# Kernel optimization log

Hardware: AMD Instinct MI355X
Metric: run time of the kernel (lower is better)

## Reference

```python
import jax, jax.numpy as jnp
import numpy as np

B, G, C, H = 32, 512, 384, 768
TAU = 0.1
ITERS = 10


def _xavier(key, shape):
    fan_in, fan_out = shape
    lim = (6.0 / (fan_in + fan_out)) ** 0.5
    return jax.random.uniform(key, shape, minval=-lim, maxval=lim, dtype=jnp.float32)


def setup_inputs() -> dict:
    key = jax.random.key(0)
    ks = jax.random.split(key, 4)
    return {
        "center_coords": jax.random.normal(ks[0], (B, G, 3), dtype=jnp.float32),
        "group_features": jax.random.normal(ks[1], (B, G, C), dtype=jnp.float32),
        "W1": _xavier(ks[2], (C, H)),
        "b1": jnp.zeros((H,), jnp.float32),
        "W2": _xavier(ks[3], (H, G)),
        "b2": jnp.zeros((G,), jnp.float32),
    }


def _sinkhorn(scores):
    # scores: (B, G, G); log-space Sinkhorn row/col normalization
    log_alpha = scores / TAU
    for _ in range(ITERS):
        log_alpha = log_alpha - jax.nn.logsumexp(log_alpha, axis=-1, keepdims=True)
        log_alpha = log_alpha - jax.nn.logsumexp(log_alpha, axis=-2, keepdims=True)
    return jnp.exp(log_alpha)


def _greedy_assign(P):
    # Equivalent to torch loop: process entries in descending value order,
    # assign (row, col) if both free == repeatedly take global argmax over
    # entries with free row and free col. P: (G, G) -> perm: (G,) int32.
    g = P.shape[-1]
    flat = P.reshape(-1)

    def step(_, carry):
        row_free, col_free, assign = carry
        mask = (row_free[:, None] & col_free[None, :]).reshape(-1)
        idx = jnp.argmax(jnp.where(mask, flat, -jnp.inf))
        r = idx // g
        c = idx % g
        return (row_free.at[r].set(False), col_free.at[c].set(False), assign.at[r].set(c.astype(jnp.int32)))

    init = (jnp.ones((g,), bool), jnp.ones((g,), bool), jnp.full((g,), -1, jnp.int32))
    _, _, assign = jax.lax.fori_loop(0, g, step, init)
    return assign


def _apply_perm(data, perm):
    # reordered[new_pos] = data[orig_pos]; perm[orig_pos] = new_pos
    return jnp.zeros_like(data).at[perm].set(data)


def reference(center_coords, group_features, W1, b1, W2, b2):
    h = jax.nn.relu(jnp.einsum('bgc,ch->bgh', group_features, W1) + b1)
    scores = jnp.einsum('bgh,hk->bgk', h, W2) + b2  # (B, G, G)
    P = _sinkhorn(scores)
    perm_indices = jax.vmap(_greedy_assign)(P)  # (B, G)
    reordered_coords = jax.vmap(_apply_perm)(center_coords, perm_indices)
    reordered_feats = jax.vmap(_apply_perm)(group_features, perm_indices)
    return reordered_coords, reordered_feats, perm_indices
```

## Files before the change

### kernel.cpp

```cpp
#include <hip/hip_runtime.h>
#include <math.h>

#define NB 32
#define NG 512
#define NC 384
#define NH 768

typedef float f32x4v __attribute__((ext_vector_type(4)));
typedef __bf16 bf16_t;
typedef bf16_t bf16x8 __attribute__((ext_vector_type(8)));
typedef bf16_t bf16x4 __attribute__((ext_vector_type(4)));

#define LDSK 32

__device__ __forceinline__ void split3(float x, bf16_t& h, bf16_t& m, bf16_t& lo)
{
    h = (bf16_t)x;
    float r1 = x - (float)h;
    m = (bf16_t)r1;
    float r2 = r1 - (float)m;
    lo = (bf16_t)r2;
}

__global__ __launch_bounds__(256, 4) void gemm_bias_mfma(
    const float* __restrict__ A, const float* __restrict__ Bw,
    const float* __restrict__ bias, float* __restrict__ Co,
    int M, int N, int K, int mode)
{
    __shared__ __align__(16) bf16_t sA[3][128][LDSK];
    __shared__ __align__(16) bf16_t sB[3][64][LDSK];
    int ntiles = N >> 6;
    int bm = (blockIdx.x / ntiles) << 7;
    int bn = (blockIdx.x % ntiles) << 6;
    int t = threadIdx.x;
    int l = t & 63;
    int w = t >> 6;
    int wr = (w >> 1) << 6;
    int wc = (w & 1) << 5;
    int fr = l & 15;
    int fk = (l >> 4) << 3;

    int sa_row = t >> 1;
    int sa_kh = (t & 1) << 4;
    int hsel = (sa_kh >> 4) << 2;
    int sb_k = (t & 7) << 2;
    int sb_n = ((t >> 3) & 15) << 2;
    bool doB = t < 128;
    int bcol = ((sb_k >> 2) & 3) * 8 + ((sb_k >> 4) << 2);

    const float* apBase = A + (size_t)(bm + sa_row) * K + sa_kh;

    f32x4v acc[4][2];
#pragma unroll
    for (int i = 0; i < 4; i++)
#pragma unroll
        for (int j = 0; j < 2; j++) acc[i][j] = (f32x4v)(0.f);

    float4 q0 = *(const float4*)(apBase + 0);
    float4 q1 = *(const float4*)(apBase + 4);
    float4 q2 = *(const float4*)(apBase + 8);
    float4 q3 = *(const float4*)(apBase + 12);
    float4 bq0, bq1, bq2, bq3;
    if (doB) {
        bq0 = *(const float4*)(Bw + (size_t)(sb_k + 0) * N + bn + sb_n);
        bq1 = *(const float4*)(Bw + (size_t)(sb_k + 1) * N + bn + sb_n);
        bq2 = *(const float4*)(Bw + (size_t)(sb_k + 2) * N + bn + sb_n);
        bq3 = *(const float4*)(Bw + (size_t)(sb_k + 3) * N + bn + sb_n);
    }

    for (int kc = 0; kc < K; kc += 32) {
        __syncthreads();
        {
            float xs[16] = { q0.x, q0.y, q0.z, q0.w, q1.x, q1.y, q1.z, q1.w,
                             q2.x, q2.y, q2.z, q2.w, q3.x, q3.y, q3.z, q3.w };
            bf16_t hs[16], ms[16], ls[16];
#pragma unroll
            for (int e = 0; e < 16; e++) split3(xs[e], hs[e], ms[e], ls[e]);
#pragma unroll
            for (int qd = 0; qd < 4; qd++) {
                int col = qd * 8 + hsel;
                *(bf16x4*)&sA[0][sa_row][col] =
                    (bf16x4){ hs[4 * qd], hs[4 * qd + 1], hs[4 * qd + 2], hs[4 * qd + 3] };
                *(bf16x4*)&sA[1][sa_row][col] =
                    (bf16x4){ ms[4 * qd], ms[4 * qd + 1], ms[4 * qd + 2], ms[4 * qd + 3] };
                *(bf16x4*)&sA[2][sa_row][col] =
                    (bf16x4){ ls[4 * qd], ls[4 * qd + 1], ls[4 * qd + 2], ls[4 * qd + 3] };
            }
        }
        if (doB) {
            float bbv[4][4] = {
                { bq0.x, bq0.y, bq0.z, bq0.w },
                { bq1.x, bq1.y, bq1.z, bq1.w },
                { bq2.x, bq2.y, bq2.z, bq2.w },
                { bq3.x, bq3.y, bq3.z, bq3.w } };
#pragma unroll
            for (int n = 0; n < 4; n++) {
                bf16_t hb[4], mb[4], lb[4];
#pragma unroll
                for (int kk = 0; kk < 4; kk++) split3(bbv[kk][n], hb[kk], mb[kk], lb[kk]);
                *(bf16x4*)&sB[0][sb_n + n][bcol] = (bf16x4){ hb[0], hb[1], hb[2], hb[3] };
                *(bf16x4*)&sB[1][sb_n + n][bcol] = (bf16x4){ mb[0], mb[1], mb[2], mb[3] };
                *(bf16x4*)&sB[2][sb_n + n][bcol] = (bf16x4){ lb[0], lb[1], lb[2], lb[3] };
            }
        }
        __syncthreads();
        if (kc + 32 < K) {
            const float* ap = apBase + kc + 32;
            q0 = *(const float4*)(ap + 0);
            q1 = *(const float4*)(ap + 4);
            q2 = *(const float4*)(ap + 8);
            q3 = *(const float4*)(ap + 12);
            if (doB) {
                const float* bp = Bw + (size_t)(kc + 32 + sb_k) * N + bn + sb_n;
                bq0 = *(const float4*)(bp + 0 * N);
                bq1 = *(const float4*)(bp + 1 * N);
                bq2 = *(const float4*)(bp + 2 * N);
                bq3 = *(const float4*)(bp + 3 * N);
            }
        }
        bf16x8 afH[4], afM[4], afL[4], bfH[2], bfM[2], bfL[2];
#pragma unroll
        for (int i = 0; i < 4; i++) {
            afH[i] = *(const bf16x8*)&sA[0][wr + i * 16 + fr][fk];
            afM[i] = *(const bf16x8*)&sA[1][wr + i * 16 + fr][fk];
            afL[i] = *(const bf16x8*)&sA[2][wr + i * 16 + fr][fk];
        }
#pragma unroll
        for (int j = 0; j < 2; j++) {
            bfH[j] = *(const bf16x8*)&sB[0][wc + j * 16 + fr][fk];
            bfM[j] = *(const bf16x8*)&sB[1][wc + j * 16 + fr][fk];
            bfL[j] = *(const bf16x8*)&sB[2][wc + j * 16 + fr][fk];
        }
#pragma unroll
        for (int i = 0; i < 4; i++)
#pragma unroll
            for (int j = 0; j < 2; j++) {
                acc[i][j] = __builtin_amdgcn_mfma_f32_16x16x32_bf16(
                    afH[i], bfH[j], acc[i][j], 0, 0, 0);
                acc[i][j] = __builtin_amdgcn_mfma_f32_16x16x32_bf16(
                    afH[i], bfM[j], acc[i][j], 0, 0, 0);
                acc[i][j] = __builtin_amdgcn_mfma_f32_16x16x32_bf16(
                    afM[i], bfH[j], acc[i][j], 0, 0, 0);
                acc[i][j] = __builtin_amdgcn_mfma_f32_16x16x32_bf16(
                    afM[i], bfM[j], acc[i][j], 0, 0, 0);
                acc[i][j] = __builtin_amdgcn_mfma_f32_16x16x32_bf16(
                    afH[i], bfL[j], acc[i][j], 0, 0, 0);
                acc[i][j] = __builtin_amdgcn_mfma_f32_16x16x32_bf16(
                    afL[i], bfH[j], acc[i][j], 0, 0, 0);
            }
    }

    int orow = (l >> 4) << 2;
#pragma unroll
    for (int j = 0; j < 2; j++) {
        int colg = bn + wc + j * 16 + fr;
        float bj = bias[colg];
#pragma unroll
        for (int i = 0; i < 4; i++) {
            int rowg = bm + wr + i * 16 + orow;
#pragma unroll
            for (int r = 0; r < 4; r++) {
                float val = acc[i][j][r] + bj;
                val = (mode == 0) ? fmaxf(val, 0.f) : val / 0.1f;
                Co[(size_t)(rowg + r) * N + colg] = val;
            }
        }
    }
}

#define DPP6_MAXF(x)                                                              \
    { int _t;                                                                     \
      _t = __builtin_amdgcn_update_dpp(__float_as_int(x), __float_as_int(x),      \
               0x111, 0xf, 0xf, false); x = fmaxf(x, __int_as_float(_t));         \
      _t = __builtin_amdgcn_update_dpp(__float_as_int(x), __float_as_int(x),      \
               0x112, 0xf, 0xf, false); x = fmaxf(x, __int_as_float(_t));         \
      _t = __builtin_amdgcn_update_dpp(__float_as_int(x), __float_as_int(x),      \
               0x114, 0xf, 0xf, false); x = fmaxf(x, __int_as_float(_t));         \
      _t = __builtin_amdgcn_update_dpp(__float_as_int(x), __float_as_int(x),      \
               0x118, 0xf, 0xf, false); x = fmaxf(x, __int_as_float(_t));         \
      _t = __builtin_amdgcn_update_dpp(__float_as_int(x), __float_as_int(x),      \
               0x142, 0xa, 0xf, false); x = fmaxf(x, __int_as_float(_t));         \
      _t = __builtin_amdgcn_update_dpp(__float_as_int(x), __float_as_int(x),      \
               0x143, 0xc, 0xf, false); x = fmaxf(x, __int_as_float(_t)); }

#define DPP6_ADDF(x)                                                              \
    { int _t;                                                                     \
      _t = __builtin_amdgcn_update_dpp(__float_as_int(x), __float_as_int(x),      \
               0x111, 0xf, 0xf, false); x = x + __int_as_float(_t);               \
      _t = __builtin_amdgcn_update_dpp(__float_as_int(x), __float_as_int(x),      \
               0x112, 0xf, 0xf, false); x = x + __int_as_float(_t);               \
      _t = __builtin_amdgcn_update_dpp(__float_as_int(x), __float_as_int(x),      \
               0x114, 0xf, 0xf, false); x = x + __int_as_float(_t);               \
      _t = __builtin_amdgcn_update_dpp(__float_as_int(x), __float_as_int(x),      \
               0x118, 0xf, 0xf, false); x = x + __int_as_float(_t);               \
      _t = __builtin_amdgcn_update_dpp(__float_as_int(x), __float_as_int(x),      \
               0x142, 0xa, 0xf, false); x = x + __int_as_float(_t);               \
      _t = __builtin_amdgcn_update_dpp(__float_as_int(x), __float_as_int(x),      \
               0x143, 0xc, 0xf, false); x = x + __int_as_float(_t); }

__global__ __launch_bounds__(256) void sinkhorn_iter(
    const float* __restrict__ A0, float* __restrict__ uu,
    const float* __restrict__ vv, float* __restrict__ ps)
{
    int blk = blockIdx.x;
    int b = blk >> 3, rc = blk & 7;
    int t = threadIdx.x;
    int l = t & 63, w = t >> 6;
    const float* vb = vv + (b << 9);
    float4 v0 = *(const float4*)(vb + 4 * l);
    float4 v1 = *(const float4*)(vb + 256 + 4 * l);
    int row0 = (rc << 6) + (w << 4);
    const float* base = A0 + ((size_t)((b << 9) + row0) << 9);

    float cs0 = 0.f, cs1 = 0.f, cs2 = 0.f, cs3 = 0.f;
    float cs4 = 0.f, cs5 = 0.f, cs6 = 0.f, cs7 = 0.f;

    for (int rr = 0; rr < 16; ++rr) {
        const float* rowp = base + ((size_t)rr << 9);
        float4 a0 = *(const float4*)(rowp + 4 * l);
        float4 a1 = *(const float4*)(rowp + 256 + 4 * l);
        float x0 = a0.x + v0.x, x1 = a0.y + v0.y;
        float x2 = a0.z + v0.z, x3 = a0.w + v0.w;
        float x4 = a1.x + v1.x, x5 = a1.y + v1.y;
        float x6 = a1.z + v1.z, x7 = a1.w + v1.w;
        float m = fmaxf(fmaxf(fmaxf(x0, x1), fmaxf(x2, x3)),
                        fmaxf(fmaxf(x4, x5), fmaxf(x6, x7)));
        DPP6_MAXF(m)
        int mi = __builtin_amdgcn_readlane(__float_as_int(m), 63);
        m = __int_as_float(mi);
        float e0 = __expf(x0 - m), e1 = __expf(x1 - m);
        float e2 = __expf(x2 - m), e3 = __expf(x3 - m);
        float e4 = __expf(x4 - m), e5 = __expf(x5 - m);
        float e6 = __expf(x6 - m), e7 = __expf(x7 - m);
        float s = ((e0 + e1) + (e2 + e3)) + ((e4 + e5) + (e6 + e7));
        DPP6_ADDF(s)
        int si = __builtin_amdgcn_readlane(__float_as_int(s), 63);
        s = __int_as_float(si);
        float inv = 1.0f / s;
        cs0 += e0 * inv; cs1 += e1 * inv; cs2 += e2 * inv; cs3 += e3 * inv;
        cs4 += e4 * inv; cs5 += e5 * inv; cs6 += e6 * inv; cs7 += e7 * inv;
        if (l == 63) uu[(b << 9) + row0 + rr] = -(m + __logf(s));
    }

    __shared__ float sacc[4][512];
    float4 w0; w0.x = cs0; w0.y = cs1; w0.z = cs2; w0.w = cs3;
    float4 w1; w1.x = cs4; w1.y = cs5; w1.z = cs6; w1.w = cs7;
    *(float4*)&sacc[w][4 * l] = w0;
    *(float4*)&sacc[w][256 + 4 * l] = w1;
    __syncthreads();
    float pA = sacc[0][t] + sacc[1][t] + sacc[2][t] + sacc[3][t];
    float pB = sacc[0][256 + t] + sacc[1][256 + t] + sacc[2][256 + t] + sacc[3][256 + t];
    int o = ((b << 3) + rc) * NG;
    ps[o + t] = pA;
    ps[o + 256 + t] = pB;
}

__global__ __launch_bounds__(256) void col_combine_lin(
    const float* __restrict__ ps, float* __restrict__ vv)
{
    int tid = blockIdx.x * 256 + threadIdx.x;
    int b = tid >> 9, j = tid & 511;
    float S = 0.f;
#pragma unroll
    for (int rc = 0; rc < 8; rc++) S += ps[((b << 3) + rc) * NG + j];
    vv[tid] = vv[tid] - __logf(S);
}

__device__ __forceinline__ void masked_row_argmax(
    const float* __restrict__ rowp, int l, unsigned int free8, int rr,
    float& outV, int& outF)
{
    float4 x0 = *(const float4*)(rowp + 8 * l);
    float4 x1 = *(const float4*)(rowp + 8 * l + 4);
    float q0 = (free8 & 1u)   ? x0.x : -1.0f;
    float q1 = (free8 & 2u)   ? x0.y : -1.0f;
    float q2 = (free8 & 4u)   ? x0.z : -1.0f;
    float q3 = (free8 & 8u)   ? x0.w : -1.0f;
    float q4 = (free8 & 16u)  ? x1.x : -1.0f;
    float q5 = (free8 & 32u)  ? x1.y : -1.0f;
    float q6 = (free8 & 64u)  ? x1.z : -1.0f;
    float q7 = (free8 & 128u) ? x1.w : -1.0f;
    float lm = fmaxf(fmaxf(fmaxf(q0, q1), fmaxf(q2, q3)),
                     fmaxf(fmaxf(q4, q5), fmaxf(q6, q7)));
    int sb = (rr << 9) + 8 * l;
    int lf = 0x7FFFFFFF;
    lf = (q7 == lm) ? sb + 7 : lf;
    lf = (q6 == lm) ? sb + 6 : lf;
    lf = (q5 == lm) ? sb + 5 : lf;
    lf = (q4 == lm) ? sb + 4 : lf;
    lf = (q3 == lm) ? sb + 3 : lf;
    lf = (q2 == lm) ? sb + 2 : lf;
    lf = (q1 == lm) ? sb + 1 : lf;
    lf = (q0 == lm) ? sb + 0 : lf;
    float gg = lm;
    DPP6_MAXF(gg)
    int ggi = __builtin_amdgcn_readlane(__float_as_int(gg), 63);
    float g1 = __int_as_float(ggi);
    unsigned long long tb = __ballot(lm == g1);
    int tl = __ffsll(tb) - 1;
    outV = g1;
    outF = __builtin_amdgcn_readlane(lf, tl);
}

__global__ __launch_bounds__(256) void p_rowmax(
    const float* __restrict__ A0, const float* __restrict__ uu,
    const float* __restrict__ vv, float* __restrict__ P,
    int* __restrict__ rbCr, int* __restrict__ rbCc,
    unsigned long long* __restrict__ freeRow,
    unsigned long long* __restrict__ freeCol,
    int* __restrict__ remaining)
{
    if (blockIdx.x == 0) {
        int t = threadIdx.x;
        freeRow[t] = ~0ULL;
        freeCol[t] = ~0ULL;
        if (t < NB) remaining[t] = NG;
    }
    int wrow = blockIdx.x * 4 + (threadIdx.x >> 6);
    int l = threadIdx.x & 63;
    int b = wrow >> 9;
    float ur = uu[wrow];
    const float* vb = vv + (b << 9);
    size_t ro = (size_t)wrow << 9;
    float4 a0 = *(const float4*)(A0 + ro + 8 * l);
    float4 a1 = *(const float4*)(A0 + ro + 8 * l + 4);
    float4 v0 = *(const float4*)(vb + 8 * l);
    float4 v1 = *(const float4*)(vb + 8 * l + 4);
    float p0 = expf(a0.x + ur + v0.x);
    float p1 = expf(a0.y + ur + v0.y);
    float p2 = expf(a0.z + ur + v0.z);
    float p3 = expf(a0.w + ur + v0.w);
    float p4 = expf(a1.x + ur + v1.x);
    float p5 = expf(a1.y + ur + v1.y);
    float p6 = expf(a1.z + ur + v1.z);
    float p7 = expf(a1.w + ur + v1.w);
    float4 o0; o0.x = p0; o0.y = p1; o0.z = p2; o0.w = p3;
    float4 o1; o1.x = p4; o1.y = p5; o1.z = p6; o1.w = p7;
    *(float4*)(P + ro + 8 * l) = o0;
    *(float4*)(P + ro + 8 * l + 4) = o1;
    float mv = fmaxf(fmaxf(fmaxf(p0, p1), fmaxf(p2, p3)),
                     fmaxf(fmaxf(p4, p5), fmaxf(p6, p7)));
    int cb = 8 * l;
    int f = 0x7FFFFFFF;
    f = (p7 == mv) ? cb + 7 : f;
    f = (p6 == mv) ? cb + 6 : f;
    f = (p5 == mv) ? cb + 5 : f;
    f = (p4 == mv) ? cb + 4 : f;
    f = (p3 == mv) ? cb + 3 : f;
    f = (p2 == mv) ? cb + 2 : f;
    f = (p1 == mv) ? cb + 1 : f;
    f = (p0 == mv) ? cb + 0 : f;
    float g = mv;
    DPP6_MAXF(g)
    int gi = __builtin_amdgcn_readlane(__float_as_int(g), 63);
    float gm = __int_as_float(gi);
    unsigned long long tb = __ballot(mv == gm);
    int tl = __ffsll(tb) - 1;
    int bestc = __builtin_amdgcn_readlane(f, tl);
    if (l == 0) { rbCr[wrow] = bestc; rbCc[wrow] = -1; }
}

__global__ __launch_bounds__(512) void mutual_round(
    const float* __restrict__ P, int* __restrict__ rbCr, int* __restrict__ rbCc,
    unsigned long long* __restrict__ freeRow,
    unsigned long long* __restrict__ freeCol,
    int* __restrict__ remaining, int* __restrict__ permInt)
{
    int b = blockIdx.x;
    if (remaining[b] == 0) return;
    int t = threadIdx.x;
    int l = t & 63;
    int w = t >> 6;
    const float* Pb = P + (size_t)b * NG * NG;

    __shared__ unsigned int fr[16], fc[16];
    __shared__ int sRC[NG];
    __shared__ int sCC[NG];
    __shared__ int freeList[NG];
    __shared__ int dirtyRows[NG];
    __shared__ int nFree, nDirtyRow, takeCnt;
    __shared__ int wCnt[8], wOff[8];

    if (t < 8) {
        unsigned long long x = freeRow[b * 8 + t];
        fr[2 * t] = (unsigned)x; fr[2 * t + 1] = (unsigned)(x >> 32);
    } else if (t < 16) {
        int i = t - 8;
        unsigned long long x = freeCol[b * 8 + i];
        fc[2 * i] = (unsigned)x; fc[2 * i + 1] = (unsigned)(x >> 32);
    }
    sRC[t] = rbCr[(b << 9) + t];
    sCC[t] = rbCc[(b << 9) + t];
    if (t == 0) { nDirtyRow = 0; takeCnt = 0; }
    __syncthreads();

    bool isFree = (fr[t >> 5] >> (t & 31)) & 1u;
    unsigned long long bm = __ballot(isFree);
    if (l == 0) wCnt[w] = __popcll(bm);
    if (isFree) {
        int c = sRC[t];
        if (!((fc[c >> 5] >> (c & 31)) & 1u)) {
            int d = atomicAdd(&nDirtyRow, 1);
            dirtyRows[d] = t;
        }
    }
    __syncthreads();
    if (t == 0) {
        int s = 0;
#pragma unroll
        for (int i = 0; i < 8; i++) { wOff[i] = s; s += wCnt[i]; }
        nFree = s;
    }
    __syncthreads();
    if (isFree) {
        int rank = __popcll(bm & ((1ULL << l) - 1ULL));
        freeList[wOff[w] + rank] = t;
    }
    __syncthreads();

    int nd = nDirtyRow;
    for (int d = w; d < nd; d += 8) {
        int r = dirtyRows[d];
        unsigned int free8 = (fc[l >> 2] >> ((l & 3) * 8)) & 0xFFu;
        float nv; int nf;
        masked_row_argmax(Pb + ((size_t)r << 9), l, free8, r, nv, nf);
        if (l == 0) {
            int c = nf & 511;
            sRC[r] = c;
            rbCr[(b << 9) + r] = c;
        }
    }
    __syncthreads();

    bool colFree = (fc[t >> 5] >> (t & 31)) & 1u;
    int cachedR = sCC[t];
    bool colDirty = colFree &&
        (cachedR < 0 || !((fr[cachedR >> 5] >> (cachedR & 31)) & 1u));
    if (colDirty) {
        float best = -1.f; int bestr = 0x7FFFFFFF;
        int nf2 = nFree;
        int i = 0;
        for (; i + 4 <= nf2; i += 4) {
            int r0 = freeList[i], r1 = freeList[i + 1];
            int r2 = freeList[i + 2], r3 = freeList[i + 3];
            float v0 = Pb[((size_t)r0 << 9) + t];
            float v1 = Pb[((size_t)r1 << 9) + t];
            float v2 = Pb[((size_t)r2 << 9) + t];
            float v3 = Pb[((size_t)r3 << 9) + t];
            if (v0 > best) { best = v0; bestr = r0; }
            if (v1 > best) { best = v1; bestr = r1; }
            if (v2 > best) { best = v2; bestr = r2; }
            if (v3 > best) { best = v3; bestr = r3; }
        }
        for (; i < nf2; ++i) {
            int ri = freeList[i];
            float vv2 = Pb[((size_t)ri << 9) + t];
            if (vv2 > best) { best = vv2; bestr = ri; }
        }
        sCC[t] = bestr;
        rbCc[(b << 9) + t] = bestr;
    }
    __syncthreads();

    if (colFree) {
        int r = sCC[t];
        if (r >= 0 && r < NG && sRC[r] == t) {
            permInt[(b << 9) + r] = t;
            atomicAnd(&fr[r >> 5], ~(1u << (r & 31)));
            atomicAnd(&fc[t >> 5], ~(1u << (t & 31)));
            atomicAdd(&takeCnt, 1);
        }
    }
    __syncthreads();
    if (t < 8) {
        freeRow[b * 8 + t] =
            ((unsigned long long)fr[2 * t + 1] << 32) | fr[2 * t];
    } else if (t < 16) {
        int i = t - 8;
        freeCol[b * 8 + i] =
            ((unsigned long long)fc[2 * i + 1] << 32) | fc[2 * i];
    }
    if (t == 0) remaining[b] = remaining[b] - takeCnt;
}

__global__ __launch_bounds__(64) void greedy_cleanup(
    const float* __restrict__ P,
    const unsigned long long* __restrict__ freeRow,
    const unsigned long long* __restrict__ freeCol,
    const int* __restrict__ remaining, int* __restrict__ permInt)
{
    int b = blockIdx.x;
    if (remaining[b] == 0) return;
    int l = threadIdx.x;
    const float* Pb = P + (size_t)b * NG * NG;

    unsigned long long wR = freeRow[b * 8 + (l >> 3)];
    unsigned int myRows = (unsigned int)((wR >> ((l & 7) * 8)) & 0xFF);
    unsigned long long wC = freeCol[b * 8 + (l >> 3)];
    unsigned int free8 = (unsigned int)((wC >> ((l & 7) * 8)) & 0xFF);

    float rv[8]; int rf[8];
#pragma unroll
    for (int k = 0; k < 8; k++) { rv[k] = -1.f; rf[k] = 0x7FFFFFFF; }

    int dmk = (int)myRows;
    unsigned long long act = __ballot(dmk != 0);
    while (act) {
        int src = __ffsll(act) - 1;
        int kk = __ffs(__builtin_amdgcn_readlane(dmk, src)) - 1;
        if (l == src) dmk &= ~(1 << kk);
        int rr = (src << 3) + kk;
        float nv; int nf;
        masked_row_argmax(Pb + ((size_t)rr << 9), l, free8, rr, nv, nf);
        bool upd = (l == src);
        rv[0] = (upd && kk == 0) ? nv : rv[0]; rf[0] = (upd && kk == 0) ? nf : rf[0];
        rv[1] = (upd && kk == 1) ? nv : rv[1]; rf[1] = (upd && kk == 1) ? nf : rf[1];
        rv[2] = (upd && kk == 2) ? nv : rv[2]; rf[2] = (upd && kk == 2) ? nf : rf[2];
        rv[3] = (upd && kk == 3) ? nv : rv[3]; rf[3] = (upd && kk == 3) ? nf : rf[3];
        rv[4] = (upd && kk == 4) ? nv : rv[4]; rf[4] = (upd && kk == 4) ? nf : rf[4];
        rv[5] = (upd && kk == 5) ? nv : rv[5]; rf[5] = (upd && kk == 5) ? nf : rf[5];
        rv[6] = (upd && kk == 6) ? nv : rv[6]; rf[6] = (upd && kk == 6) ? nf : rf[6];
        rv[7] = (upd && kk == 7) ? nv : rv[7]; rf[7] = (upd && kk == 7) ? nf : rf[7];
        act = __ballot(dmk != 0);
    }

    for (int step = 0; step < NG; ++step) {
        float mv = fmaxf(fmaxf(fmaxf(rv[0], rv[1]), fmaxf(rv[2], rv[3])),
                         fmaxf(fmaxf(rv[4], rv[5]), fmaxf(rv[6], rv[7])));
        int f = 0x7FFFFFFF;
        f = (rv[7] == mv) ? rf[7] : f;
        f = (rv[6] == mv) ? rf[6] : f;
        f = (rv[5] == mv) ? rf[5] : f;
        f = (rv[4] == mv) ? rf[4] : f;
        f = (rv[3] == mv) ? rf[3] : f;
        f = (rv[2] == mv) ? rf[2] : f;
        f = (rv[1] == mv) ? rf[1] : f;
        f = (rv[0] == mv) ? rf[0] : f;
        float g = mv;
        DPP6_MAXF(g)
        int gi = __builtin_amdgcn_readlane(__float_as_int(g), 63);
        float gm = __int_as_float(gi);
        if (gm < 0.f) break;
        unsigned long long tb = __ballot(mv == gm);
        int tl = __ffsll(tb) - 1;
        int bestf = __builtin_amdgcn_readlane(f, tl);
        int r = bestf >> 9, c = bestf & 511;
        if (l == 0) permInt[(b << 9) + r] = c;
        if (l == (c >> 3)) free8 &= ~(1u << (c & 7));
        int rl = r - (l << 3);
        int dm2 = 0;
#pragma unroll
        for (int k = 0; k < 8; k++) {
            bool alive = rv[k] >= 0.f;
            bool cm = ((rf[k] ^ c) & 511) == 0;
            bool taken = (rl == k);
            if (taken) rv[k] = -1.f;
            dm2 |= (alive && cm && !taken) ? (1 << k) : 0;
        }
        unsigned long long act2 = __ballot(dm2 != 0);
        while (act2) {
            int src = __ffsll(act2) - 1;
            int kk = __ffs(__builtin_amdgcn_readlane(dm2, src)) - 1;
            if (l == src) dm2 &= ~(1 << kk);
            int rr = (src << 3) + kk;
            float nv; int nf;
            masked_row_argmax(Pb + ((size_t)rr << 9), l, free8, rr, nv, nf);
            bool upd = (l == src);
            rv[0] = (upd && kk == 0) ? nv : rv[0]; rf[0] = (upd && kk == 0) ? nf : rf[0];
            rv[1] = (upd && kk == 1) ? nv : rv[1]; rf[1] = (upd && kk == 1) ? nf : rf[1];
            rv[2] = (upd && kk == 2) ? nv : rv[2]; rf[2] = (upd && kk == 2) ? nf : rf[2];
            rv[3] = (upd && kk == 3) ? nv : rv[3]; rf[3] = (upd && kk == 3) ? nf : rf[3];
            rv[4] = (upd && kk == 4) ? nv : rv[4]; rf[4] = (upd && kk == 4) ? nf : rf[4];
            rv[5] = (upd && kk == 5) ? nv : rv[5]; rf[5] = (upd && kk == 5) ? nf : rf[5];
            rv[6] = (upd && kk == 6) ? nv : rv[6]; rf[6] = (upd && kk == 6) ? nf : rf[6];
            rv[7] = (upd && kk == 7) ? nv : rv[7]; rf[7] = (upd && kk == 7) ? nf : rf[7];
            act2 = __ballot(dm2 != 0);
        }
    }
}

__global__ void scatter_all(const float* __restrict__ coords,
    const float* __restrict__ feats, const int* __restrict__ perm,
    float* __restrict__ dstCoords, float* __restrict__ dstFeats,
    float* __restrict__ permF)
{
    int tid = blockIdx.x * 256 + threadIdx.x;
    int rc = tid / 96;
    int q = tid - rc * 96;
    int b = rc >> 9;
    int p = perm[rc];
    const float4* s4 = (const float4*)(feats + (size_t)rc * NC);
    float4* d4 = (float4*)(dstFeats + ((size_t)(b << 9) + p) * NC);
    d4[q] = s4[q];
    if (q == 0) {
        permF[rc] = (float)p;
        size_t so = (size_t)rc * 3;
        size_t dd = ((size_t)(b << 9) + p) * 3;
        dstCoords[dd] = coords[so];
        dstCoords[dd + 1] = coords[so + 1];
        dstCoords[dd + 2] = coords[so + 2];
    }
}

extern "C" void kernel_launch(void* const* d_in, const int* in_sizes, int n_in,
                              void* d_out, int out_size, void* d_ws, size_t ws_size,
                              hipStream_t stream)
{
    const float* coords = (const float*)d_in[0];
    const float* feats  = (const float*)d_in[1];
    const float* W1 = (const float*)d_in[2];
    const float* b1 = (const float*)d_in[3];
    const float* W2 = (const float*)d_in[4];
    const float* b2 = (const float*)d_in[5];

    float* out = (float*)d_out;
    float* outCoords = out;
    float* outFeats  = out + (size_t)NB * NG * 3;
    float* outPerm   = out + (size_t)NB * NG * 3 + (size_t)NB * NG * NC;

    float* ws = (float*)d_ws;
    float* h   = ws;
    float* A0  = h + (size_t)NB * NG * NH;
    float* u   = A0 + (size_t)NB * NG * NG;
    float* v   = u + NB * NG;
    float* pm  = v + NB * NG;
    float* ps  = pm + NB * 8 * NG;
    int* rbCr  = (int*)(ps + NB * 8 * NG);
    int* rbCc  = rbCr + NB * NG;
    unsigned long long* freeRow = (unsigned long long*)(rbCc + NB * NG);
    unsigned long long* freeCol = freeRow + NB * 8;
    int* remaining = (int*)(freeCol + NB * 8);
    int* permInt   = remaining + 32;

    const int M = NB * NG;

    gemm_bias_mfma<<<dim3((M / 128) * (NH / 64)), 256, 0, stream>>>(
        feats, W1, b1, h, M, NH, NC, 0);
    gemm_bias_mfma<<<dim3((M / 128) * (NG / 64)), 256, 0, stream>>>(
        h, W2, b2, A0, M, NG, NH, 1);

    hipMemsetAsync(v, 0, (size_t)NB * NG * sizeof(float), stream);

    for (int it = 0; it < 10; ++it) {
        sinkhorn_iter<<<dim3(NB * 8), 256, 0, stream>>>(A0, u, v, ps);
        col_combine_lin<<<dim3(M / 256), 256, 0, stream>>>(ps, v);
    }

    float* P = h;
    p_rowmax<<<dim3(M / 4), 256, 0, stream>>>(A0, u, v, P, rbCr, rbCc,
                                              freeRow, freeCol, remaining);

    for (int r = 0; r < 6; ++r)
        mutual_round<<<dim3(NB), 512, 0, stream>>>(P, rbCr, rbCc, freeRow,
                                                   freeCol, remaining, permInt);

    greedy_cleanup<<<dim3(NB), 64, 0, stream>>>(P, freeRow, freeCol,
                                                remaining, permInt);

    scatter_all<<<dim3((NB * NG * 96) / 256), 256, 0, stream>>>(
        coords, feats, permInt, outCoords, outFeats, outPerm);
}
```

Before: 425.0 us.

## Swizzle GEMM LDS layout and fuse Sinkhorn column combine into row pass

The GEMM's shared-memory tiles for A and B now use an XOR swizzle on the k-slot, keyed on the row index, to cut LDS bank conflicts on the fragment reads. The separate column-combine kernel is folded into the next Sinkhorn iteration: each block rebuilds the column potentials from the previous partial sums into shared memory, using ping-pong v and partial-sum buffers. This drops about nine kernel launches, but every block in a batch now redundantly recomputes the 512-entry column reduction.

New measurement: 403.0 us. 1.05x faster.

```diff
diff --git a/kernel.cpp b/kernel.cpp
--- a/kernel.cpp
+++ b/kernel.cpp
@@ -38,15 +38,17 @@
     int wr = (w >> 1) << 6;
     int wc = (w & 1) << 5;
     int fr = l & 15;
-    int fk = (l >> 4) << 3;
+    int fq = l >> 4;
 
     int sa_row = t >> 1;
     int sa_kh = (t & 1) << 4;
     int hsel = (sa_kh >> 4) << 2;
+    int aswz = (sa_row >> 1) & 3;
     int sb_k = (t & 7) << 2;
     int sb_n = ((t >> 3) & 15) << 2;
     bool doB = t < 128;
-    int bcol = ((sb_k >> 2) & 3) * 8 + ((sb_k >> 4) << 2);
+    int bslot = (sb_k >> 2) & 3;
+    int bsub = (sb_k >> 4) << 2;
 
     const float* apBase = A + (size_t)(bm + sa_row) * K + sa_kh;
 
@@ -78,7 +80,7 @@
             for (int e = 0; e < 16; e++) split3(xs[e], hs[e], ms[e], ls[e]);
 #pragma unroll
             for (int qd = 0; qd < 4; qd++) {
-                int col = qd * 8 + hsel;
+                int col = ((qd ^ aswz) << 3) + hsel;
                 *(bf16x4*)&sA[0][sa_row][col] =
                     (bf16x4){ hs[4 * qd], hs[4 * qd + 1], hs[4 * qd + 2], hs[4 * qd + 3] };
                 *(bf16x4*)&sA[1][sa_row][col] =
@@ -95,12 +97,14 @@
                 { bq3.x, bq3.y, bq3.z, bq3.w } };
 #pragma unroll
             for (int n = 0; n < 4; n++) {
+                int rb = sb_n + n;
+                int col = ((bslot ^ ((rb >> 1) & 3)) << 3) + bsub;
                 bf16_t hb[4], mb[4], lb[4];
 #pragma unroll
                 for (int kk = 0; kk < 4; kk++) split3(bbv[kk][n], hb[kk], mb[kk], lb[kk]);
-                *(bf16x4*)&sB[0][sb_n + n][bcol] = (bf16x4){ hb[0], hb[1], hb[2], hb[3] };
-                *(bf16x4*)&sB[1][sb_n + n][bcol] = (bf16x4){ mb[0], mb[1], mb[2], mb[3] };
-                *(bf16x4*)&sB[2][sb_n + n][bcol] = (bf16x4){ lb[0], lb[1], lb[2], lb[3] };
+                *(bf16x4*)&sB[0][rb][col] = (bf16x4){ hb[0], hb[1], hb[2], hb[3] };
+                *(bf16x4*)&sB[1][rb][col] = (bf16x4){ mb[0], mb[1], mb[2], mb[3] };
+                *(bf16x4*)&sB[2][rb][col] = (bf16x4){ lb[0], lb[1], lb[2], lb[3] };
             }
         }
         __syncthreads();
@@ -121,15 +125,19 @@
         bf16x8 afH[4], afM[4], afL[4], bfH[2], bfM[2], bfL[2];
 #pragma unroll
         for (int i = 0; i < 4; i++) {
-            afH[i] = *(const bf16x8*)&sA[0][wr + i * 16 + fr][fk];
-            afM[i] = *(const bf16x8*)&sA[1][wr + i * 16 + fr][fk];
-            afL[i] = *(const bf16x8*)&sA[2][wr + i * 16 + fr][fk];
+            int ra = wr + i * 16 + fr;
+            int pk = ((fq ^ ((ra >> 1) & 3)) << 3);
+            afH[i] = *(const bf16x8*)&sA[0][ra][pk];
+            afM[i] = *(const bf16x8*)&sA[1][ra][pk];
+            afL[i] = *(const bf16x8*)&sA[2][ra][pk];
         }
 #pragma unroll
         for (int j = 0; j < 2; j++) {
-            bfH[j] = *(const bf16x8*)&sB[0][wc + j * 16 + fr][fk];
-            bfM[j] = *(const bf16x8*)&sB[1][wc + j * 16 + fr][fk];
-            bfL[j] = *(const bf16x8*)&sB[2][wc + j * 16 + fr][fk];
+            int rb = wc + j * 16 + fr;
+            int pk = ((fq ^ ((rb >> 1) & 3)) << 3);
+            bfH[j] = *(const bf16x8*)&sB[0][rb][pk];
+            bfM[j] = *(const bf16x8*)&sB[1][rb][pk];
+            bfL[j] = *(const bf16x8*)&sB[2][rb][pk];
         }
 #pragma unroll
         for (int i = 0; i < 4; i++)
@@ -150,7 +158,7 @@
             }
     }
 
-    int orow = (l >> 4) << 2;
+    int orow = fq << 2;
 #pragma unroll
     for (int j = 0; j < 2; j++) {
         int colg = bn + wc + j * 16 + fr;
@@ -198,17 +206,36 @@
       _t = __builtin_amdgcn_update_dpp(__float_as_int(x), __float_as_int(x),      \
                0x143, 0xc, 0xf, false); x = x + __int_as_float(_t); }
 
-__global__ __launch_bounds__(256) void sinkhorn_iter(
+__global__ __launch_bounds__(256) void sinkhorn_iter_fused(
     const float* __restrict__ A0, float* __restrict__ uu,
-    const float* __restrict__ vv, float* __restrict__ ps)
+    const float* __restrict__ vIn, float* __restrict__ vOut,
+    const float* __restrict__ psIn, float* __restrict__ psOut, int first)
 {
     int blk = blockIdx.x;
     int b = blk >> 3, rc = blk & 7;
     int t = threadIdx.x;
     int l = t & 63, w = t >> 6;
-    const float* vb = vv + (b << 9);
-    float4 v0 = *(const float4*)(vb + 4 * l);
-    float4 v1 = *(const float4*)(vb + 256 + 4 * l);
+    __shared__ __align__(16) float svv[512];
+
+    if (first) {
+        svv[t] = 0.f;
+        svv[256 + t] = 0.f;
+    } else {
+#pragma unroll
+        for (int h2 = 0; h2 < 2; h2++) {
+            int j = h2 * 256 + t;
+            float S = 0.f;
+#pragma unroll
+            for (int r8 = 0; r8 < 8; r8++) S += psIn[((b << 3) + r8) * NG + j];
+            float nv = vIn[(b << 9) + j] - __logf(S);
+            svv[j] = nv;
+            if (rc == 0) vOut[(b << 9) + j] = nv;
+        }
+    }
+    __syncthreads();
+
+    float4 v0 = *(const float4*)(&svv[4 * l]);
+    float4 v1 = *(const float4*)(&svv[256 + 4 * l]);
     int row0 = (rc << 6) + (w << 4);
     const float* base = A0 + ((size_t)((b << 9) + row0) << 9);
 
@@ -251,19 +278,20 @@
     float pA = sacc[0][t] + sacc[1][t] + sacc[2][t] + sacc[3][t];
     float pB = sacc[0][256 + t] + sacc[1][256 + t] + sacc[2][256 + t] + sacc[3][256 + t];
     int o = ((b << 3) + rc) * NG;
-    ps[o + t] = pA;
-    ps[o + 256 + t] = pB;
-}
-
-__global__ __launch_bounds__(256) void col_combine_lin(
-    const float* __restrict__ ps, float* __restrict__ vv)
+    psOut[o + t] = pA;
+    psOut[o + 256 + t] = pB;
+}
+
+__global__ __launch_bounds__(256) void col_combine_final(
+    const float* __restrict__ psIn, const float* __restrict__ vIn,
+    float* __restrict__ vOut)
 {
     int tid = blockIdx.x * 256 + threadIdx.x;
     int b = tid >> 9, j = tid & 511;
     float S = 0.f;
 #pragma unroll
-    for (int rc = 0; rc < 8; rc++) S += ps[((b << 3) + rc) * NG + j];
-    vv[tid] = vv[tid] - __logf(S);
+    for (int r8 = 0; r8 < 8; r8++) S += psIn[((b << 3) + r8) * NG + j];
+    vOut[tid] = vIn[tid] - __logf(S);
 }
 
 __device__ __forceinline__ void masked_row_argmax(
@@ -622,15 +650,16 @@
     float* h   = ws;
     float* A0  = h + (size_t)NB * NG * NH;
     float* u   = A0 + (size_t)NB * NG * NG;
-    float* v   = u + NB * NG;
-    float* pm  = v + NB * NG;
-    float* ps  = pm + NB * 8 * NG;
-    int* rbCr  = (int*)(ps + NB * 8 * NG);
+    float* vA  = u + NB * NG;
+    float* ps0 = vA + NB * NG;
+    float* ps1 = ps0 + NB * 8 * NG;
+    int* rbCr  = (int*)(ps1 + NB * 8 * NG);
     int* rbCc  = rbCr + NB * NG;
     unsigned long long* freeRow = (unsigned long long*)(rbCc + NB * NG);
     unsigned long long* freeCol = freeRow + NB * 8;
     int* remaining = (int*)(freeCol + NB * 8);
     int* permInt   = remaining + 32;
+    float* vB  = (float*)(permInt + NB * NG);
 
     const int M = NB * NG;
 
@@ -639,15 +668,21 @@
     gemm_bias_mfma<<<dim3((M / 128) * (NG / 64)), 256, 0, stream>>>(
         h, W2, b2, A0, M, NG, NH, 1);
 
-    hipMemsetAsync(v, 0, (size_t)NB * NG * sizeof(float), stream);
-
-    for (int it = 0; it < 10; ++it) {
-        sinkhorn_iter<<<dim3(NB * 8), 256, 0, stream>>>(A0, u, v, ps);
-        col_combine_lin<<<dim3(M / 256), 256, 0, stream>>>(ps, v);
-    }
+    hipMemsetAsync(vA, 0, (size_t)NB * NG * sizeof(float), stream);
+
+    float* pbuf[2] = { ps0, ps1 };
+    for (int i = 1; i <= 10; ++i) {
+        const float* vin = (i % 2 == 0) ? vA : vB;
+        float* vout      = (i % 2 == 0) ? vB : vA;
+        const float* pin = pbuf[i & 1];
+        float* pout      = pbuf[(i - 1) & 1];
+        sinkhorn_iter_fused<<<dim3(NB * 8), 256, 0, stream>>>(
+            A0, u, vin, vout, pin, pout, (i == 1) ? 1 : 0);
+    }
+    col_combine_final<<<dim3(M / 256), 256, 0, stream>>>(pbuf[1], vB, vA);
 
     float* P = h;
-    p_rowmax<<<dim3(M / 4), 256, 0, stream>>>(A0, u, v, P, rbCr, rbCc,
+    p_rowmax<<<dim3(M / 4), 256, 0, stream>>>(A0, u, vA, P, rbCr, rbCc,
                                               freeRow, freeCol, remaining);
 
     for (int r = 0; r < 6; ++r)
```
